# Optimization experiments

Measured on AMD Instinct MI355X. Metric: run time of the kernel, lower is better.

Reference implementation:

```python
import jax, jax.numpy as jnp
import numpy as np

# Module hyperparameters (from __init__ defaults / init_kwargs)
A_PLUS = 0.005
A_MINUS = 0.00525
TAU_PLUS = 20.0
TAU_MINUS = 20.0
DT = 1.0

B, T, N_PRE, N_POST = 512, 100, 256, 256
SPIKE_RATE = 0.1


def setup_inputs() -> dict:
    key = jax.random.key(0)
    k1, k2, k3 = jax.random.split(key, 3)
    pre_spikes = (jax.random.uniform(k1, (B, T, N_PRE)) < SPIKE_RATE).astype(jnp.float32)
    post_spikes = (jax.random.uniform(k2, (B, T, N_POST)) < SPIKE_RATE).astype(jnp.float32)
    weights = jax.random.uniform(k3, (N_PRE, N_POST), dtype=jnp.float32)
    return {"pre_spikes": pre_spikes, "post_spikes": post_spikes, "weights": weights}


def _pre_trace(pre_tbn, decay):
    """trace[t] = sum_{tau=1..t} decay^tau * pre[t-tau]  (exact recurrence).

    pre_tbn: [T, B, N]. Returns [T, B, N] with trace[0] = 0.
    """
    def step(carry, x_t):
        # emit trace[t] = carry, then carry' = decay * (carry + pre[t])
        return decay * (carry + x_t), carry
    _, trace = jax.lax.scan(step, jnp.zeros_like(pre_tbn[0]), pre_tbn)
    return trace


def reference(pre_spikes, post_spikes, weights):
    """Classical STDP weight update.

    With T <= int(tau_plus*5) the original nested t/tau loops equal:
      dW[p,q] = (1/(B*T)) * sum_{t,b} (A+ * trace+[t,b,p] - A- * trace-[t,b,p]) * post[b,t,q]
    where trace+/- are exponential pre-synaptic eligibility traces.
    """
    batch, time_steps, _ = pre_spikes.shape
    pre_t = jnp.transpose(pre_spikes, (1, 0, 2))    # [T, B, n_pre]
    post_t = jnp.transpose(post_spikes, (1, 0, 2))  # [T, B, n_post]

    decay_plus = jnp.exp(jnp.float32(-DT / TAU_PLUS))
    decay_minus = jnp.exp(jnp.float32(-DT / TAU_MINUS))

    trace_plus = _pre_trace(pre_t, decay_plus)    # LTP: pre fires before post
    trace_minus = _pre_trace(pre_t, decay_minus)  # LTD: pre fires before post (depression of reversed pairing)

    eff = A_PLUS * trace_plus - A_MINUS * trace_minus  # [T, B, n_pre]
    weight_update = jnp.einsum('tbp,tbq->pq', eff, post_t) / (batch * time_steps)
    # original initializes update as zeros_like(weights); output shape matches weights
    return weight_update + jnp.zeros_like(weights)
```

## Files before the change

kernel.cpp:

```cpp
#include <hip/hip_runtime.h>
#include <stdint.h>

#define B_SZ   512
#define T_SZ   100
#define NPRE   256
#define NPOST  256
#define KTOT   (B_SZ * T_SZ)

typedef __bf16 bf16x8 __attribute__((ext_vector_type(8)));
typedef float  floatx4 __attribute__((ext_vector_type(4)));

__device__ __forceinline__ uint32_t pack_rne2(float a_done, uint32_t lo) {
    (void)a_done; return lo;
}
__device__ __forceinline__ uint32_t bf16_rne(float v) {
    uint32_t bits = __float_as_uint(v);
    return (bits + 0x7FFFu + ((bits >> 16) & 1u)) >> 16;
}
__device__ __forceinline__ uint32_t pack_trunc2(float a, float b) {
    return (__float_as_uint(a) >> 16) | (__float_as_uint(b) & 0xFFFF0000u);
}

__global__ __launch_bounds__(256) void stdp_trace_prep(
    const float* __restrict__ pre, unsigned short* __restrict__ trace_t)
{
    __shared__ __align__(16) unsigned short T_lds[4][256][8];

    const int b = blockIdx.x;
    const int p = threadIdx.x;
    const int lane = p & 63, wave = p >> 6;
    const float decay = 0.95122942450071400910f;
    const float* src = pre + (size_t)b * (T_SZ * NPRE) + p;

    float carry = 0.0f;
    for (int kc = 0; kc < 4; ++kc) {
        uint32_t pk[16];
        if (kc < 3) {
            float x[32];
#pragma unroll
            for (int j = 0; j < 32; ++j)
                x[j] = src[(size_t)(kc * 32 + j) * NPRE];
#pragma unroll
            for (int j = 0; j < 16; ++j) {
                uint32_t lo = bf16_rne(carry);
                carry = decay * (carry + x[2 * j]);
                uint32_t hi = bf16_rne(carry);
                carry = decay * (carry + x[2 * j + 1]);
                pk[j] = lo | (hi << 16);
            }
        } else {
            float x[4];
#pragma unroll
            for (int j = 0; j < 4; ++j)
                x[j] = src[(size_t)(96 + j) * NPRE];
#pragma unroll
            for (int j = 0; j < 2; ++j) {
                uint32_t lo = bf16_rne(carry);
                carry = decay * (carry + x[2 * j]);
                uint32_t hi = bf16_rne(carry);
                carry = decay * (carry + x[2 * j + 1]);
                pk[j] = lo | (hi << 16);
            }
#pragma unroll
            for (int j = 2; j < 16; ++j) pk[j] = 0u;
        }
#pragma unroll
        for (int o = 0; o < 4; ++o)
            *(uint4*)&T_lds[o][p][0] =
                make_uint4(pk[o * 4], pk[o * 4 + 1], pk[o * 4 + 2], pk[o * 4 + 3]);
        __syncthreads();
#pragma unroll
        for (int i = 0; i < 4; ++i) {
            int pg = wave * 4 + i;
            uint4 v = *(const uint4*)&T_lds[lane >> 4][pg * 16 + (lane & 15)][0];
            *(uint4*)(trace_t + (((size_t)(b * 4 + kc) * 16 + pg) << 9) + lane * 8) = v;
        }
        __syncthreads();
    }
}

__global__ __launch_bounds__(512) void stdp_gemm(
    const unsigned short* __restrict__ trace_t,
    const float* __restrict__ post,
    float* __restrict__ partial)
{
    __shared__ __align__(16) unsigned short B_lds[64][512];

    const int bx = blockIdx.x;
    const int s  = bx >> 1;
    const int pt = bx & 1;
    const int tid = threadIdx.x;
    const int lane = tid & 63, wave = tid >> 6;
    const int wp = wave & 3, wq = wave >> 2;
    const int l15 = lane & 15, l4 = lane >> 4;

    const int q = tid & 255, hh = tid >> 8;
    const int qg = q >> 4, q15 = q & 15;

    floatx4 acc[2][8] = {};

    for (int lb = 0; lb < 4; ++lb) {
        const int b = s * 4 + lb;

        bf16x8 a_pf[4][2];
#pragma unroll
        for (int kc = 0; kc < 4; ++kc)
#pragma unroll
            for (int f = 0; f < 2; ++f) {
                int pg = pt * 8 + wp * 2 + f;
                a_pf[kc][f] = *(const bf16x8*)(
                    trace_t + (((size_t)(b * 4 + kc) * 16 + pg) << 9) + lane * 8);
            }

        const float* pb = post + (size_t)b * (T_SZ * NPOST) + q;
        if (hh == 0) {
#pragma unroll
            for (int half = 0; half < 2; ++half) {
                float x[32];
#pragma unroll
                for (int j = 0; j < 32; ++j)
                    x[j] = pb[(size_t)(half * 32 + j) * NPOST];
#pragma unroll
                for (int o = 0; o < 4; ++o) {
                    int oct = half * 4 + o;
                    uint4 v = make_uint4(pack_trunc2(x[o * 8 + 0], x[o * 8 + 1]),
                                         pack_trunc2(x[o * 8 + 2], x[o * 8 + 3]),
                                         pack_trunc2(x[o * 8 + 4], x[o * 8 + 5]),
                                         pack_trunc2(x[o * 8 + 6], x[o * 8 + 7]));
                    *(uint4*)&B_lds[(oct >> 2) * 16 + qg][(((oct & 3) * 16 + q15)) * 8] = v;
                }
            }
        } else {
            float x[32];
#pragma unroll
            for (int j = 0; j < 32; ++j)
                x[j] = pb[(size_t)(64 + j) * NPOST];
            float y[4];
#pragma unroll
            for (int j = 0; j < 4; ++j)
                y[j] = pb[(size_t)(96 + j) * NPOST];
#pragma unroll
            for (int o = 0; o < 4; ++o) {
                int oct = 8 + o;
                uint4 v = make_uint4(pack_trunc2(x[o * 8 + 0], x[o * 8 + 1]),
                                     pack_trunc2(x[o * 8 + 2], x[o * 8 + 3]),
                                     pack_trunc2(x[o * 8 + 4], x[o * 8 + 5]),
                                     pack_trunc2(x[o * 8 + 6], x[o * 8 + 7]));
                *(uint4*)&B_lds[(oct >> 2) * 16 + qg][(((oct & 3) * 16 + q15)) * 8] = v;
            }
            {
                uint4 v = make_uint4(pack_trunc2(y[0], y[1]),
                                     pack_trunc2(y[2], y[3]), 0u, 0u);
                *(uint4*)&B_lds[3 * 16 + qg][((0 * 16 + q15)) * 8] = v;
            }
#pragma unroll
            for (int o = 13; o < 16; ++o)
                *(uint4*)&B_lds[3 * 16 + qg][(((o & 3) * 16 + q15)) * 8] =
                    make_uint4(0u, 0u, 0u, 0u);
        }
        __syncthreads();

#pragma unroll
        for (int kc = 0; kc < 4; ++kc) {
            bf16x8 bb[8];
#pragma unroll
            for (int g = 0; g < 8; ++g)
                bb[g] = *(const bf16x8*)&B_lds[kc * 16 + wq * 8 + g][lane * 8];
#pragma unroll
            for (int f = 0; f < 2; ++f)
#pragma unroll
                for (int g = 0; g < 8; ++g)
                    acc[f][g] = __builtin_amdgcn_mfma_f32_16x16x32_bf16(
                        a_pf[kc][f], bb[g], acc[f][g], 0, 0, 0);
        }
        __syncthreads();
    }

    float* pout = partial + (size_t)bx * (128 * 256);
#pragma unroll
    for (int f = 0; f < 2; ++f) {
        int r0 = wp * 32 + f * 16 + l4 * 4;
#pragma unroll
        for (int g = 0; g < 8; ++g) {
            int c = wq * 128 + g * 16 + l15;
#pragma unroll
            for (int v = 0; v < 4; ++v)
                pout[(size_t)(r0 + v) * 256 + c] = acc[f][g][v];
        }
    }
}

__global__ __launch_bounds__(256) void stdp_reduce(
    const float* __restrict__ partial, float* __restrict__ out)
{
    const int idx = blockIdx.x * 256 + threadIdx.x;
    const int P = idx >> 8, Q = idx & 255;
    const float* src = partial + (size_t)(P >> 7) * 32768 +
                       (size_t)(P & 127) * 256 + Q;
    float a8[8] = {};
#pragma unroll
    for (int i = 0; i < 16; ++i)
#pragma unroll
        for (int u = 0; u < 8; ++u)
            a8[u] += src[(size_t)((u * 16 + i) * 2) * 32768];
    float sum = ((a8[0] + a8[1]) + (a8[2] + a8[3])) +
                ((a8[4] + a8[5]) + (a8[6] + a8[7]));
    const float scale = (0.005f - 0.00525f) * (1.0f / (float)KTOT);
    out[idx] = sum * scale;
}

extern "C" void kernel_launch(void* const* d_in, const int* in_sizes, int n_in,
                              void* d_out, int out_size, void* d_ws, size_t ws_size,
                              hipStream_t stream)
{
    const float* pre  = (const float*)d_in[0];
    const float* post = (const float*)d_in[1];
    float* out = (float*)d_out;

    unsigned short* trace_t = (unsigned short*)d_ws;
    float* partial = (float*)((char*)d_ws + (size_t)33554432);

    stdp_trace_prep<<<512, 256, 0, stream>>>(pre, trace_t);
    stdp_gemm<<<256, 512, 0, stream>>>(trace_t, post, partial);
    stdp_reduce<<<256, 256, 0, stream>>>(partial, out);
}
```

Measured before the change: 151.9 us.

## Split partial-sum reduction into two stages and remap GEMM block indexing

The single reduction kernel, which ran only 256 blocks each summing 128 partials per output, becomes a two-stage reduction. The first stage uses 2048 blocks to sum 16 partials each into a temporary buffer, and the second sums 8 values per output. This is meant to expose more parallelism and memory-level concurrency when reading the 32 MB partial buffer. The GEMM block index mapping also changes so that consecutive blocks cover different batch slices rather than the two p-halves of the same slice. That changes L2 sharing of the post loads. The cost is an extra launch and a temporary-buffer round trip.

```diff
diff --git a/kernel.cpp b/kernel.cpp
--- a/kernel.cpp
+++ b/kernel.cpp
@@ -10,9 +10,6 @@
 typedef __bf16 bf16x8 __attribute__((ext_vector_type(8)));
 typedef float  floatx4 __attribute__((ext_vector_type(4)));
 
-__device__ __forceinline__ uint32_t pack_rne2(float a_done, uint32_t lo) {
-    (void)a_done; return lo;
-}
 __device__ __forceinline__ uint32_t bf16_rne(float v) {
     uint32_t bits = __float_as_uint(v);
     return (bits + 0x7FFFu + ((bits >> 16) & 1u)) >> 16;
@@ -87,8 +84,8 @@
     __shared__ __align__(16) unsigned short B_lds[64][512];
 
     const int bx = blockIdx.x;
-    const int s  = bx >> 1;
-    const int pt = bx & 1;
+    const int s  = bx & 127;
+    const int pt = bx >> 7;
     const int tid = threadIdx.x;
     const int lane = tid & 63, wave = tid >> 6;
     const int wp = wave & 3, wq = wave >> 2;
@@ -148,11 +145,8 @@
                                      pack_trunc2(x[o * 8 + 6], x[o * 8 + 7]));
                 *(uint4*)&B_lds[(oct >> 2) * 16 + qg][(((oct & 3) * 16 + q15)) * 8] = v;
             }
-            {
-                uint4 v = make_uint4(pack_trunc2(y[0], y[1]),
-                                     pack_trunc2(y[2], y[3]), 0u, 0u);
-                *(uint4*)&B_lds[3 * 16 + qg][((0 * 16 + q15)) * 8] = v;
-            }
+            *(uint4*)&B_lds[3 * 16 + qg][(q15) * 8] =
+                make_uint4(pack_trunc2(y[0], y[1]), pack_trunc2(y[2], y[3]), 0u, 0u);
 #pragma unroll
             for (int o = 13; o < 16; ++o)
                 *(uint4*)&B_lds[3 * 16 + qg][(((o & 3) * 16 + q15)) * 8] =
@@ -190,23 +184,34 @@
     }
 }
 
-__global__ __launch_bounds__(256) void stdp_reduce(
-    const float* __restrict__ partial, float* __restrict__ out)
+__global__ __launch_bounds__(256) void stdp_reduce1(
+    const float* __restrict__ partial, float* __restrict__ tmp)
+{
+    const int t = blockIdx.x * 256 + threadIdx.x;
+    const int g = t >> 16;
+    const int e = t & 65535;
+    const int pt = e >> 15;
+    const float* src = partial + ((size_t)(pt * 128 + g * 16)) * 32768 + (e & 32767);
+    float a4[4] = {};
+#pragma unroll
+    for (int i = 0; i < 4; ++i)
+#pragma unroll
+        for (int u = 0; u < 4; ++u)
+            a4[u] += src[(size_t)(u * 4 + i) * 32768];
+    tmp[t] = (a4[0] + a4[1]) + (a4[2] + a4[3]);
+}
+
+__global__ __launch_bounds__(256) void stdp_reduce2(
+    const float* __restrict__ tmp, float* __restrict__ out)
 {
     const int idx = blockIdx.x * 256 + threadIdx.x;
-    const int P = idx >> 8, Q = idx & 255;
-    const float* src = partial + (size_t)(P >> 7) * 32768 +
-                       (size_t)(P & 127) * 256 + Q;
-    float a8[8] = {};
-#pragma unroll
-    for (int i = 0; i < 16; ++i)
-#pragma unroll
-        for (int u = 0; u < 8; ++u)
-            a8[u] += src[(size_t)((u * 16 + i) * 2) * 32768];
-    float sum = ((a8[0] + a8[1]) + (a8[2] + a8[3])) +
-                ((a8[4] + a8[5]) + (a8[6] + a8[7]));
+    float a[4];
+#pragma unroll
+    for (int u = 0; u < 4; ++u)
+        a[u] = tmp[(size_t)(2 * u) * 65536 + idx] +
+               tmp[(size_t)(2 * u + 1) * 65536 + idx];
     const float scale = (0.005f - 0.00525f) * (1.0f / (float)KTOT);
-    out[idx] = sum * scale;
+    out[idx] = ((a[0] + a[1]) + (a[2] + a[3])) * scale;
 }
 
 extern "C" void kernel_launch(void* const* d_in, const int* in_sizes, int n_in,
@@ -219,8 +224,10 @@
 
     unsigned short* trace_t = (unsigned short*)d_ws;
     float* partial = (float*)((char*)d_ws + (size_t)33554432);
+    float* tmp     = (float*)((char*)d_ws + (size_t)67108864);
 
     stdp_trace_prep<<<512, 256, 0, stream>>>(pre, trace_t);
     stdp_gemm<<<256, 512, 0, stream>>>(trace_t, post, partial);
-    stdp_reduce<<<256, 256, 0, stream>>>(partial, out);
-}
+    stdp_reduce1<<<2048, 256, 0, stream>>>(partial, tmp);
+    stdp_reduce2<<<256, 256, 0, stream>>>(tmp, out);
+}
```

New measurement: 153.7 us. About the same (+1.2%).
